# Performance work log

Measured on AMD Instinct MI355X. Metric: run time of the kernel, lower is better.

Reference implementation:

```python
import jax, jax.numpy as jnp
import numpy as np
import math

B, L, E, H = 4, 2048, 1024, 16
HD = E // H
SIGMA = 10.0
ATTN_BIAS = 0.1  # source bug: dropout_p=0.1 is passed as attn_mask and added to scores


def setup_inputs() -> dict:
    key = jax.random.key(0)
    ks = jax.random.split(key, 6)
    return {
        "query": jax.random.normal(ks[0], (B, L, E), jnp.float32),
        "key": jax.random.normal(ks[1], (B, L, E), jnp.float32),
        "value": jax.random.normal(ks[2], (B, L, E), jnp.float32),
        "gauss": jax.random.uniform(ks[3], (B * H // 2, L), jnp.float32),
        "in_proj_weight": jax.random.normal(ks[4], (3 * E, E), jnp.float32) * (1.0 / math.sqrt(E)),
        "in_proj_bias": jnp.zeros((3 * E,), jnp.float32),
        "out_proj_weight": jax.random.normal(ks[5], (E, E), jnp.float32) * (1.0 / math.sqrt(E)),
        "out_proj_bias": jnp.zeros((E,), jnp.float32),
    }


def reference(query, key, value, gauss, in_proj_weight, in_proj_bias,
              out_proj_weight, out_proj_bias):
    # packed in-projection (q,k,v distinct tensors -> chunk weights in 3)
    wq, wk, wv = jnp.split(in_proj_weight, 3, axis=0)   # each [E, E]
    bq, bk, bv = jnp.split(in_proj_bias, 3, axis=0)
    q = query @ wq.T + bq          # [B, L, E]
    k = key @ wk.T + bk
    v = value @ wv.T + bv

    def split_heads(x):            # [B, L, E] -> [B*H, L, HD], index = b*H + h
        return x.reshape(B, L, H, HD).transpose(0, 2, 1, 3).reshape(B * H, L, HD)

    q, k, v = split_heads(q), split_heads(k), split_heads(v)
    q = q * (1.0 / math.sqrt(HD))

    attn = jnp.einsum("bnd,bmd->bnm", q, k) + ATTN_BIAS   # [B*H, L, L]
    gw = jnp.exp(-gauss * SIGMA)                          # [B*H//2, L]
    # even/odd batch rows share the same gaussian row -> pairwise broadcast
    attn = (attn.reshape(B * H // 2, 2, L, L) * gw[:, None, None, :]).reshape(B * H, L, L)
    attn = jax.nn.softmax(attn, axis=-1)

    out = jnp.einsum("bnm,bmd->bnd", attn, v)             # [B*H, L, HD]
    out = out.reshape(B, H, L, HD).transpose(0, 2, 1, 3).reshape(B, L, E)
    return out @ out_proj_weight.T + out_proj_bias        # [B, L, E]
```

## Files before the change

### kernel.cpp

```cpp
#include <hip/hip_runtime.h>
#include <stdint.h>
#include <stddef.h>


typedef __attribute__((ext_vector_type(8))) short bf16x8;
typedef __attribute__((ext_vector_type(4))) float f32x4;
typedef __attribute__((ext_vector_type(8))) float f32x8;

__device__ __forceinline__ unsigned short f2b(float f) {
  unsigned int u = __builtin_bit_cast(unsigned int, f);
  u += 0x7FFFu + ((u >> 16) & 1u);
  return (unsigned short)(u >> 16);
}
__device__ __forceinline__ bf16x8 cvt8(f32x4 a, f32x4 b) {
  bf16x8 r;
#pragma unroll
  for (int i = 0; i < 4; ++i) { r[i] = (short)f2b(a[i]); r[4 + i] = (short)f2b(b[i]); }
  return r;
}
__device__ __forceinline__ bf16x8 pk8(f32x4 a, f32x4 b) {
  union { bf16x8 v; unsigned int w[4]; } u;
  asm("v_cvt_pk_bf16_f32 %0, %1, %2" : "=v"(u.w[0]) : "v"(a[0]), "v"(a[1]));
  asm("v_cvt_pk_bf16_f32 %0, %1, %2" : "=v"(u.w[1]) : "v"(a[2]), "v"(a[3]));
  asm("v_cvt_pk_bf16_f32 %0, %1, %2" : "=v"(u.w[2]) : "v"(b[0]), "v"(b[1]));
  asm("v_cvt_pk_bf16_f32 %0, %1, %2" : "=v"(u.w[3]) : "v"(b[2]), "v"(b[3]));
  return u.v;
}
__device__ __forceinline__ float fexp2(float x) { return __builtin_amdgcn_exp2f(x); }

#define GLD16(gp, lp) __builtin_amdgcn_global_load_lds( \
  (const __attribute__((address_space(1))) void*)(gp), \
  (__attribute__((address_space(3))) void*)(lp), 16, 0, 0)

__global__ void __launch_bounds__(256) gw_exp_kernel(const float* __restrict__ g,
                                                     float* __restrict__ gw2, int n) {
  int i = blockIdx.x * 256 + threadIdx.x;
  if (i < n) {
    const float e = __expf(g[i] * -10.0f) * 1.44269504f;
    gw2[2 * i] = e;
    gw2[2 * i + 1] = 0.1f * e;
  }
}

__global__ void __launch_bounds__(256) conv_bf16_kernel(
    const float* __restrict__ q, const float* __restrict__ k, const float* __restrict__ v,
    const float* __restrict__ w1, const float* __restrict__ w2,
    unsigned short* __restrict__ dst)
{
  const size_t i = ((size_t)blockIdx.x * 256 + threadIdx.x) * 8;
  const int seg = (int)(i >> 20);
  const float* s; size_t off;
  if (seg < 8)       { s = q;  off = i; }
  else if (seg < 16) { s = k;  off = i - ((size_t)8 << 20); }
  else if (seg < 24) { s = v;  off = i - ((size_t)16 << 20); }
  else if (seg < 27) { s = w1; off = i - ((size_t)24 << 20); }
  else               { s = w2; off = i - ((size_t)27 << 20); }
  const f32x4 a = *(const f32x4*)(s + off);
  const f32x4 b = *(const f32x4*)(s + off + 4);
  *(bf16x8*)(dst + i) = cvt8(a, b);
}

template<int EPI>
__global__ void __launch_bounds__(512) gemm_bt(
    const unsigned short* __restrict__ A0, const unsigned short* __restrict__ Bw,
    const float* __restrict__ bias,
    unsigned short* __restrict__ Qo, unsigned short* __restrict__ Ko,
    unsigned short* __restrict__ Vto, float* __restrict__ Co,
    int N, int K, int nTN)
{
  const int nwg = gridDim.x;
  const int cpx = nwg >> 3;
  const int bid2 = (blockIdx.x & 7) * cpx + (blockIdx.x >> 3);
  const int tm = bid2 / nTN, tn = bid2 % nTN;

  const unsigned short* A = A0;
  if (EPI == 0) A = A0 + (size_t)(tn >> 3) * 8388608;

  __shared__ __align__(16) char lds[3][16384];

  const int tid = threadIdx.x;
  const int w = tid >> 6, l = tid & 63;
  const int lr = l & 15, lg = l >> 4;
  const size_t Kz = (size_t)K;

  auto stage = [&](int buf, int kt) {
    const int k0 = kt * 32;
    const int rl = l >> 2;
    const int cs = (l & 3) ^ ((l >> 3) & 3);
    const size_t row = (size_t)(w * 16 + rl);
    GLD16(A  + Kz * (tm * 128 + row) + k0 + cs * 8, &lds[buf][w * 1024]);
    GLD16(Bw + Kz * (tn * 128 + row) + k0 + cs * 8, &lds[buf][8192 + w * 1024]);
  };

  auto loadFrag = [&](const char* ld, int row) -> bf16x8 {
    return *(const bf16x8*)(ld + row * 64 + ((lg ^ ((row >> 1) & 3)) << 4));
  };

  f32x4 acc[4][2];
  const f32x4 zero = {0.f, 0.f, 0.f, 0.f};
#pragma unroll
  for (int i = 0; i < 4; ++i)
#pragma unroll
    for (int j = 0; j < 2; ++j) acc[i][j] = zero;

  const int wr = (w >> 2) * 64, wc = (w & 3) * 32;
  const int NT = K / 32;

  stage(0, 0);
  stage(1, 1);
  int rb = 0, wb = 2;
  for (int kt = 0; kt < NT; ++kt) {
    if (kt == NT - 1) { asm volatile("s_waitcnt vmcnt(0)" ::: "memory"); }
    else              { asm volatile("s_waitcnt vmcnt(2)" ::: "memory"); }
    __builtin_amdgcn_sched_barrier(0);
    __builtin_amdgcn_s_barrier();
    __builtin_amdgcn_sched_barrier(0);
    if (kt + 2 < NT) stage(wb, kt + 2);
    const char* la = lds[rb];
    const char* lb = lds[rb] + 8192;
    bf16x8 af[4], bfr[2];
#pragma unroll
    for (int mi = 0; mi < 4; ++mi) af[mi] = loadFrag(la, wr + mi * 16 + lr);
#pragma unroll
    for (int ni = 0; ni < 2; ++ni) bfr[ni] = loadFrag(lb, wc + ni * 16 + lr);
#pragma unroll
    for (int mi = 0; mi < 4; ++mi)
#pragma unroll
      for (int ni = 0; ni < 2; ++ni)
        acc[mi][ni] = __builtin_amdgcn_mfma_f32_16x16x32_bf16(
            af[mi], bfr[ni], acc[mi][ni], 0, 0, 0);
    rb = (rb == 2) ? 0 : rb + 1;
    wb = (wb == 2) ? 0 : wb + 1;
  }

  if (EPI == 0 && tn >= 16) {
    __syncthreads();
    char* T = &lds[0][0];
#pragma unroll
    for (int ni = 0; ni < 2; ++ni) {
      const int cnl = wc + ni * 16 + lr;
      const float bv = bias[tn * 128 + cnl];
#pragma unroll
      for (int mi = 0; mi < 4; ++mi)
#pragma unroll
        for (int r = 0; r < 4; ++r) {
          const int rml = wr + mi * 16 + lg * 4 + r;
          const int byte = cnl * 256 + (((rml * 2)) ^ ((cnl & 3) << 5));
          *(unsigned short*)(T + byte) = f2b(acc[mi][ni][r] + bv);
        }
    }
    __syncthreads();
    const int bbase = (tm >> 4) * 16 + (tn - 16) * 2;
    const size_t ncol = (size_t)(tm & 15) * 128;
#pragma unroll
    for (int rep = 0; rep < 4; ++rep) {
      const int U = rep * 512 + tid;
      const int row = U >> 4;
      const int un = U & 15;
      const bf16x8 vv = *(const bf16x8*)(T + row * 256 + ((un * 16) ^ ((row & 3) << 5)));
      const int bh = bbase + (row >> 6);
      const int d = row & 63;
      *(bf16x8*)(Vto + ((size_t)bh * 64 + d) * 2048 + ncol + un * 8) = vv;
    }
  } else {
#pragma unroll
    for (int ni = 0; ni < 2; ++ni) {
      const int cn = tn * 128 + wc + ni * 16 + lr;
      const float bv = bias[cn];
#pragma unroll
      for (int mi = 0; mi < 4; ++mi) {
#pragma unroll
        for (int r = 0; r < 4; ++r) {
          const int rm = tm * 128 + wr + mi * 16 + lg * 4 + r;
          const float val = acc[mi][ni][r] + bv;
          if constexpr (EPI == 0) {
            const int which = cn >> 10;
            const int j = cn & 1023;
            const int bh = (rm >> 11) * 16 + (j >> 6);
            const int d = j & 63;
            const int n = rm & 2047;
            if (which == 0) Qo[((size_t)bh * 2048 + n) * 64 + d] = f2b(val * 0.125f);
            else            Ko[((size_t)bh * 2048 + n) * 64 + d] = f2b(val);
          } else {
            Co[(size_t)rm * N + cn] = val;
          }
        }
      }
    }
  }
}

__global__ void __launch_bounds__(256, 4) attn_kernel(
    const unsigned short* __restrict__ Q, const unsigned short* __restrict__ Kf,
    const unsigned short* __restrict__ Vt, const float* __restrict__ gw2,
    unsigned short* __restrict__ O)
{
  const int bh = blockIdx.x >> 4;
  const int qb = blockIdx.x & 15;
  const int tid = threadIdx.x;
  const int w = tid >> 6, l = tid & 63;
  const int lr = l & 15, lg = l >> 4;

  __shared__ __align__(16) unsigned short Kl[2][64 * 64];
  __shared__ __align__(16) unsigned short Vl[2][64 * 64];

  const int qrow = qb * 128 + w * 32 + lr;
  const unsigned short* qp = &Q[((size_t)bh * 2048 + qrow) * 64];
  const bf16x8 aqA0 = *(const bf16x8*)&qp[lg * 8];
  const bf16x8 aqA1 = *(const bf16x8*)&qp[32 + lg * 8];
  const bf16x8 aqB0 = *(const bf16x8*)&qp[16 * 64 + lg * 8];
  const bf16x8 aqB1 = *(const bf16x8*)&qp[16 * 64 + 32 + lg * 8];

  const f32x4 zero = {0.f, 0.f, 0.f, 0.f};
  f32x4 accOA[4], accOB[4], lA = zero, lB = zero;
#pragma unroll
  for (int dt = 0; dt < 4; ++dt) { accOA[dt] = zero; accOB[dt] = zero; }

  const short oneb = (short)0x3F80;
  const bf16x8 vones = {oneb, oneb, oneb, oneb, oneb, oneb, oneb, oneb};

  int off[4][2];
#pragma unroll
  for (int mt = 0; mt < 4; ++mt)
#pragma unroll
    for (int c = 0; c < 2; ++c) {
      const int rr = mt * 16 + lr;
      off[mt][c] = rr * 128 + ((((c << 2) + lg) ^ (rr & 7)) << 4);
    }

  const int rr0 = w * 8 + (l >> 3);
  const int cc = ((l & 7) ^ (rr0 & 7)) * 8;
  const int kk0 = (rr0 & 35) | ((rr0 & 12) << 1) | ((rr0 & 16) >> 2);
  const unsigned short* kSrc = &Kf[((size_t)bh * 2048 + kk0) * 64 + cc];
  const unsigned short* vSrc = &Vt[((size_t)bh * 64 + rr0) * 2048 + cc];

  auto stageKV = [&](int buf) {
    GLD16(kSrc,             &Kl[buf][w * 512]);
    GLD16(kSrc + 32 * 64,   &Kl[buf][(w + 4) * 512]);
    GLD16(vSrc,             &Vl[buf][w * 512]);
    GLD16(vSrc + 32 * 2048, &Vl[buf][(w + 4) * 512]);
    kSrc += 64 * 64;
    vSrc += 64;
  };

  const float* gwrow = &gw2[(size_t)(bh >> 1) * 4096];

  stageKV(0);
  for (int t = 0; t < 32; ++t) {
    __syncthreads();
    if (t + 1 < 32) stageKV((t + 1) & 1);
    const char* kl = (const char*)Kl[t & 1];
    const char* vl = (const char*)Vl[t & 1];

    f32x4 s0[4], s1[4];
    __builtin_amdgcn_s_setprio(1);
#pragma unroll
    for (int mt = 0; mt < 4; ++mt) {
      f32x4 a0 = zero, a1 = zero;
#pragma unroll
      for (int dk = 0; dk < 2; ++dk) {
        const bf16x8 bk = *(const bf16x8*)(kl + off[mt][dk]);
        a0 = __builtin_amdgcn_mfma_f32_16x16x32_bf16(bk, dk ? aqA1 : aqA0, a0, 0, 0, 0);
        a1 = __builtin_amdgcn_mfma_f32_16x16x32_bf16(bk, dk ? aqB1 : aqB0, a1, 0, 0, 0);
      }
      const f32x8 g8 = *(const f32x8*)(gwrow + ((t << 7) + ((mt >> 1) << 6) + ((mt & 1) << 3) + (lg << 4)));
#pragma unroll
      for (int r = 0; r < 4; ++r) {
        s0[mt][r] = __builtin_fmaf(a0[r], g8[2 * r], g8[2 * r + 1]);
        s1[mt][r] = __builtin_fmaf(a1[r], g8[2 * r], g8[2 * r + 1]);
      }
    }
    __builtin_amdgcn_s_setprio(0);

#pragma unroll
    for (int mt = 0; mt < 4; ++mt)
#pragma unroll
      for (int r = 0; r < 4; ++r) {
        s0[mt][r] = fexp2(s0[mt][r]);
        s1[mt][r] = fexp2(s1[mt][r]);
      }
    const bf16x8 apA0 = pk8(s0[0], s0[1]);
    const bf16x8 apA1 = pk8(s0[2], s0[3]);
    const bf16x8 apB0 = pk8(s1[0], s1[1]);
    const bf16x8 apB1 = pk8(s1[2], s1[3]);

    __builtin_amdgcn_s_setprio(1);
    lA = __builtin_amdgcn_mfma_f32_16x16x32_bf16(apA0, vones, lA, 0, 0, 0);
    lA = __builtin_amdgcn_mfma_f32_16x16x32_bf16(apA1, vones, lA, 0, 0, 0);
    lB = __builtin_amdgcn_mfma_f32_16x16x32_bf16(apB0, vones, lB, 0, 0, 0);
    lB = __builtin_amdgcn_mfma_f32_16x16x32_bf16(apB1, vones, lB, 0, 0, 0);

#pragma unroll
    for (int dt = 0; dt < 4; ++dt) {
      f32x4 a = accOA[dt], b = accOB[dt];
#pragma unroll
      for (int ms = 0; ms < 2; ++ms) {
        const bf16x8 bv = *(const bf16x8*)(vl + off[dt][ms]);
        a = __builtin_amdgcn_mfma_f32_16x16x32_bf16(ms ? apA1 : apA0, bv, a, 0, 0, 0);
        b = __builtin_amdgcn_mfma_f32_16x16x32_bf16(ms ? apB1 : apB0, bv, b, 0, 0, 0);
      }
      accOA[dt] = a; accOB[dt] = b;
    }
    __builtin_amdgcn_s_setprio(0);
  }

  const int orowA = (bh >> 4) * 2048 + qb * 128 + w * 32 + lg * 4;
  const int oc0 = (bh & 15) * 64;
  f32x4 rA, rB;
#pragma unroll
  for (int r = 0; r < 4; ++r) { rA[r] = 1.0f / lA[r]; rB[r] = 1.0f / lB[r]; }
#pragma unroll
  for (int dt = 0; dt < 4; ++dt) {
#pragma unroll
    for (int r = 0; r < 4; ++r) {
      O[(size_t)(orowA + r) * 1024 + oc0 + dt * 16 + lr]      = f2b(accOA[dt][r] * rA[r]);
      O[(size_t)(orowA + 16 + r) * 1024 + oc0 + dt * 16 + lr] = f2b(accOB[dt][r] * rB[r]);
    }
  }
}

extern "C" void kernel_launch(void* const* d_in, const int* in_sizes, int n_in,
                              void* d_out, int out_size, void* d_ws, size_t ws_size,
                              hipStream_t stream) {
  (void)in_sizes; (void)n_in; (void)out_size; (void)ws_size;
  const float* query = (const float*)d_in[0];
  const float* key_  = (const float*)d_in[1];
  const float* value = (const float*)d_in[2];
  const float* gauss = (const float*)d_in[3];
  const float* ipw   = (const float*)d_in[4];
  const float* ipb   = (const float*)d_in[5];
  const float* opw   = (const float*)d_in[6];
  const float* opb   = (const float*)d_in[7];

  char* ws = (char*)d_ws;
  unsigned short* Xbf = (unsigned short*)ws;
  unsigned short* W1  = Xbf + ((size_t)24 << 20);
  unsigned short* W2  = Xbf + ((size_t)27 << 20);
  unsigned short* AO  = Xbf;
  unsigned short* Qf  = Xbf + ((size_t)28 << 20);
  unsigned short* Kf  = Qf + (size_t)64 * 2048 * 64;
  unsigned short* Vt  = Kf + (size_t)64 * 2048 * 64;
  float*          gw2 = (float*)(Vt + (size_t)64 * 2048 * 64);

  gw_exp_kernel<<<256, 256, 0, stream>>>(gauss, gw2, 32 * 2048);

  conv_bf16_kernel<<<14336, 256, 0, stream>>>(query, key_, value, ipw, opw, Xbf);

  gemm_bt<0><<<64 * 24, 512, 0, stream>>>(
      Xbf, W1, ipb, Qf, Kf, Vt, nullptr, 3072, 1024, 24);

  attn_kernel<<<64 * 16, 256, 0, stream>>>(Qf, Kf, Vt, gw2, AO);

  gemm_bt<1><<<64 * 8, 512, 0, stream>>>(
      AO, W2, opb, nullptr, nullptr, nullptr, (float*)d_out, 1024, 1024, 8);
}
```

Baseline: 210.5 us.

## Fold gaussian scale into K projection and double attention rows per wave

The per-key gaussian weight (with log2e) is now multiplied into K inside the QKV projection epilogue, and the remaining additive bias is fed directly as the MFMA accumulator init. This removes the per-score FMA and interleaved table loads from the attention loop. Each wave now handles 64 query rows instead of 32, so every K/V fragment read from LDS is reused across four subtiles, with grid remapping and launch bounds lowered to 2 to allow the larger register footprint. The costs are more registers per thread, lower occupancy, and K rounded to bf16 after the gaussian scaling.

```diff
diff --git a/kernel.cpp b/kernel.cpp
--- a/kernel.cpp
+++ b/kernel.cpp
@@ -5,7 +5,6 @@
 
 typedef __attribute__((ext_vector_type(8))) short bf16x8;
 typedef __attribute__((ext_vector_type(4))) float f32x4;
-typedef __attribute__((ext_vector_type(8))) float f32x8;
 
 __device__ __forceinline__ unsigned short f2b(float f) {
   unsigned int u = __builtin_bit_cast(unsigned int, f);
@@ -33,12 +32,13 @@
   (__attribute__((address_space(3))) void*)(lp), 16, 0, 0)
 
 __global__ void __launch_bounds__(256) gw_exp_kernel(const float* __restrict__ g,
-                                                     float* __restrict__ gw2, int n) {
+                                                     float* __restrict__ gtab,
+                                                     float* __restrict__ btab, int n) {
   int i = blockIdx.x * 256 + threadIdx.x;
   if (i < n) {
     const float e = __expf(g[i] * -10.0f) * 1.44269504f;
-    gw2[2 * i] = e;
-    gw2[2 * i + 1] = 0.1f * e;
+    gtab[i] = e;
+    btab[i] = 0.1f * e;
   }
 }
 
@@ -63,7 +63,7 @@
 template<int EPI>
 __global__ void __launch_bounds__(512) gemm_bt(
     const unsigned short* __restrict__ A0, const unsigned short* __restrict__ Bw,
-    const float* __restrict__ bias,
+    const float* __restrict__ bias, const float* __restrict__ gtab,
     unsigned short* __restrict__ Qo, unsigned short* __restrict__ Ko,
     unsigned short* __restrict__ Vto, float* __restrict__ Co,
     int N, int K, int nTN)
@@ -167,20 +167,32 @@
     for (int ni = 0; ni < 2; ++ni) {
       const int cn = tn * 128 + wc + ni * 16 + lr;
       const float bv = bias[cn];
+      const int j = cn & 1023;
+      const float* gK = nullptr;
+      if constexpr (EPI == 0) {
+        if ((cn >> 10) == 1) {
+          const int bh_ = (tm >> 4) * 16 + (j >> 6);
+          gK = gtab + (size_t)(bh_ >> 1) * 2048;
+        }
+      }
 #pragma unroll
       for (int mi = 0; mi < 4; ++mi) {
+        const int rm0 = tm * 128 + wr + mi * 16 + lg * 4;
+        f32x4 g4;
+        if constexpr (EPI == 0) {
+          if (gK) g4 = *(const f32x4*)&gK[rm0 & 2047];
+        }
 #pragma unroll
         for (int r = 0; r < 4; ++r) {
-          const int rm = tm * 128 + wr + mi * 16 + lg * 4 + r;
+          const int rm = rm0 + r;
           const float val = acc[mi][ni][r] + bv;
           if constexpr (EPI == 0) {
             const int which = cn >> 10;
-            const int j = cn & 1023;
             const int bh = (rm >> 11) * 16 + (j >> 6);
             const int d = j & 63;
             const int n = rm & 2047;
             if (which == 0) Qo[((size_t)bh * 2048 + n) * 64 + d] = f2b(val * 0.125f);
-            else            Ko[((size_t)bh * 2048 + n) * 64 + d] = f2b(val);
+            else            Ko[((size_t)bh * 2048 + n) * 64 + d] = f2b(val * g4[r]);
           } else {
             Co[(size_t)rm * N + cn] = val;
           }
@@ -190,13 +202,14 @@
   }
 }
 
-__global__ void __launch_bounds__(256, 4) attn_kernel(
+__global__ void __launch_bounds__(256, 2) attn_kernel(
     const unsigned short* __restrict__ Q, const unsigned short* __restrict__ Kf,
-    const unsigned short* __restrict__ Vt, const float* __restrict__ gw2,
+    const unsigned short* __restrict__ Vt, const float* __restrict__ btab,
     unsigned short* __restrict__ O)
 {
-  const int bh = blockIdx.x >> 4;
-  const int qb = blockIdx.x & 15;
+  const int bid2 = (blockIdx.x & 7) * 64 + (blockIdx.x >> 3);
+  const int bh = bid2 >> 3;
+  const int qb = bid2 & 7;
   const int tid = threadIdx.x;
   const int w = tid >> 6, l = tid & 63;
   const int lr = l & 15, lg = l >> 4;
@@ -204,17 +217,24 @@
   __shared__ __align__(16) unsigned short Kl[2][64 * 64];
   __shared__ __align__(16) unsigned short Vl[2][64 * 64];
 
-  const int qrow = qb * 128 + w * 32 + lr;
+  const int qrow = qb * 256 + w * 64 + lr;
   const unsigned short* qp = &Q[((size_t)bh * 2048 + qrow) * 64];
-  const bf16x8 aqA0 = *(const bf16x8*)&qp[lg * 8];
-  const bf16x8 aqA1 = *(const bf16x8*)&qp[32 + lg * 8];
-  const bf16x8 aqB0 = *(const bf16x8*)&qp[16 * 64 + lg * 8];
-  const bf16x8 aqB1 = *(const bf16x8*)&qp[16 * 64 + 32 + lg * 8];
+  bf16x8 aq[4][2];
+#pragma unroll
+  for (int st = 0; st < 4; ++st) {
+    aq[st][0] = *(const bf16x8*)&qp[st * 16 * 64 + lg * 8];
+    aq[st][1] = *(const bf16x8*)&qp[st * 16 * 64 + 32 + lg * 8];
+  }
 
   const f32x4 zero = {0.f, 0.f, 0.f, 0.f};
-  f32x4 accOA[4], accOB[4], lA = zero, lB = zero;
-#pragma unroll
-  for (int dt = 0; dt < 4; ++dt) { accOA[dt] = zero; accOB[dt] = zero; }
+  f32x4 accO[4][4];
+  f32x4 lsum[4];
+#pragma unroll
+  for (int st = 0; st < 4; ++st) {
+    lsum[st] = zero;
+#pragma unroll
+    for (int dt = 0; dt < 4; ++dt) accO[st][dt] = zero;
+  }
 
   const short oneb = (short)0x3F80;
   const bf16x8 vones = {oneb, oneb, oneb, oneb, oneb, oneb, oneb, oneb};
@@ -243,7 +263,7 @@
     vSrc += 64;
   };
 
-  const float* gwrow = &gw2[(size_t)(bh >> 1) * 4096];
+  const float* brow = &btab[(size_t)(bh >> 1) * 2048];
 
   stageKV(0);
   for (int t = 0; t < 32; ++t) {
@@ -252,70 +272,68 @@
     const char* kl = (const char*)Kl[t & 1];
     const char* vl = (const char*)Vl[t & 1];
 
-    f32x4 s0[4], s1[4];
+    bf16x8 ap[4][2];
+#pragma unroll
+    for (int half = 0; half < 2; ++half) {
+      f32x4 s[4][2];
+      __builtin_amdgcn_s_setprio(1);
+#pragma unroll
+      for (int mh = 0; mh < 2; ++mh) {
+        const int mt = half * 2 + mh;
+        const bf16x8 bk0 = *(const bf16x8*)(kl + off[mt][0]);
+        const bf16x8 bk1 = *(const bf16x8*)(kl + off[mt][1]);
+        const f32x4 b4 = *(const f32x4*)&brow[t * 64 + (half << 5) + (lg << 3) + (mh << 2)];
+#pragma unroll
+        for (int st = 0; st < 4; ++st) {
+          f32x4 a = __builtin_amdgcn_mfma_f32_16x16x32_bf16(bk0, aq[st][0], b4, 0, 0, 0);
+          a = __builtin_amdgcn_mfma_f32_16x16x32_bf16(bk1, aq[st][1], a, 0, 0, 0);
+          s[st][mh] = a;
+        }
+      }
+      __builtin_amdgcn_s_setprio(0);
+#pragma unroll
+      for (int st = 0; st < 4; ++st) {
+#pragma unroll
+        for (int mh = 0; mh < 2; ++mh)
+#pragma unroll
+          for (int r = 0; r < 4; ++r) s[st][mh][r] = fexp2(s[st][mh][r]);
+        ap[st][half] = pk8(s[st][0], s[st][1]);
+      }
+    }
+
     __builtin_amdgcn_s_setprio(1);
 #pragma unroll
-    for (int mt = 0; mt < 4; ++mt) {
-      f32x4 a0 = zero, a1 = zero;
-#pragma unroll
-      for (int dk = 0; dk < 2; ++dk) {
-        const bf16x8 bk = *(const bf16x8*)(kl + off[mt][dk]);
-        a0 = __builtin_amdgcn_mfma_f32_16x16x32_bf16(bk, dk ? aqA1 : aqA0, a0, 0, 0, 0);
-        a1 = __builtin_amdgcn_mfma_f32_16x16x32_bf16(bk, dk ? aqB1 : aqB0, a1, 0, 0, 0);
-      }
-      const f32x8 g8 = *(const f32x8*)(gwrow + ((t << 7) + ((mt >> 1) << 6) + ((mt & 1) << 3) + (lg << 4)));
-#pragma unroll
-      for (int r = 0; r < 4; ++r) {
-        s0[mt][r] = __builtin_fmaf(a0[r], g8[2 * r], g8[2 * r + 1]);
-        s1[mt][r] = __builtin_fmaf(a1[r], g8[2 * r], g8[2 * r + 1]);
+    for (int st = 0; st < 4; ++st) {
+      lsum[st] = __builtin_amdgcn_mfma_f32_16x16x32_bf16(ap[st][0], vones, lsum[st], 0, 0, 0);
+      lsum[st] = __builtin_amdgcn_mfma_f32_16x16x32_bf16(ap[st][1], vones, lsum[st], 0, 0, 0);
+    }
+#pragma unroll
+    for (int dt = 0; dt < 4; ++dt) {
+      const bf16x8 bv0 = *(const bf16x8*)(vl + off[dt][0]);
+      const bf16x8 bv1 = *(const bf16x8*)(vl + off[dt][1]);
+#pragma unroll
+      for (int st = 0; st < 4; ++st) {
+        f32x4 a = accO[st][dt];
+        a = __builtin_amdgcn_mfma_f32_16x16x32_bf16(ap[st][0], bv0, a, 0, 0, 0);
+        a = __builtin_amdgcn_mfma_f32_16x16x32_bf16(ap[st][1], bv1, a, 0, 0, 0);
+        accO[st][dt] = a;
       }
     }
     __builtin_amdgcn_s_setprio(0);
-
-#pragma unroll
-    for (int mt = 0; mt < 4; ++mt)
-#pragma unroll
-      for (int r = 0; r < 4; ++r) {
-        s0[mt][r] = fexp2(s0[mt][r]);
-        s1[mt][r] = fexp2(s1[mt][r]);
-      }
-    const bf16x8 apA0 = pk8(s0[0], s0[1]);
-    const bf16x8 apA1 = pk8(s0[2], s0[3]);
-    const bf16x8 apB0 = pk8(s1[0], s1[1]);
-    const bf16x8 apB1 = pk8(s1[2], s1[3]);
-
-    __builtin_amdgcn_s_setprio(1);
-    lA = __builtin_amdgcn_mfma_f32_16x16x32_bf16(apA0, vones, lA, 0, 0, 0);
-    lA = __builtin_amdgcn_mfma_f32_16x16x32_bf16(apA1, vones, lA, 0, 0, 0);
-    lB = __builtin_amdgcn_mfma_f32_16x16x32_bf16(apB0, vones, lB, 0, 0, 0);
-    lB = __builtin_amdgcn_mfma_f32_16x16x32_bf16(apB1, vones, lB, 0, 0, 0);
-
-#pragma unroll
-    for (int dt = 0; dt < 4; ++dt) {
-      f32x4 a = accOA[dt], b = accOB[dt];
-#pragma unroll
-      for (int ms = 0; ms < 2; ++ms) {
-        const bf16x8 bv = *(const bf16x8*)(vl + off[dt][ms]);
-        a = __builtin_amdgcn_mfma_f32_16x16x32_bf16(ms ? apA1 : apA0, bv, a, 0, 0, 0);
-        b = __builtin_amdgcn_mfma_f32_16x16x32_bf16(ms ? apB1 : apB0, bv, b, 0, 0, 0);
-      }
-      accOA[dt] = a; accOB[dt] = b;
-    }
-    __builtin_amdgcn_s_setprio(0);
-  }
-
-  const int orowA = (bh >> 4) * 2048 + qb * 128 + w * 32 + lg * 4;
+  }
+
   const int oc0 = (bh & 15) * 64;
-  f32x4 rA, rB;
-#pragma unroll
-  for (int r = 0; r < 4; ++r) { rA[r] = 1.0f / lA[r]; rB[r] = 1.0f / lB[r]; }
-#pragma unroll
-  for (int dt = 0; dt < 4; ++dt) {
-#pragma unroll
-    for (int r = 0; r < 4; ++r) {
-      O[(size_t)(orowA + r) * 1024 + oc0 + dt * 16 + lr]      = f2b(accOA[dt][r] * rA[r]);
-      O[(size_t)(orowA + 16 + r) * 1024 + oc0 + dt * 16 + lr] = f2b(accOB[dt][r] * rB[r]);
-    }
+#pragma unroll
+  for (int st = 0; st < 4; ++st) {
+    const int orow0 = (bh >> 4) * 2048 + qb * 256 + w * 64 + st * 16 + lg * 4;
+    f32x4 rc;
+#pragma unroll
+    for (int r = 0; r < 4; ++r) rc[r] = 1.0f / lsum[st][r];
+#pragma unroll
+    for (int dt = 0; dt < 4; ++dt)
+#pragma unroll
+      for (int r = 0; r < 4; ++r)
+        O[(size_t)(orow0 + r) * 1024 + oc0 + dt * 16 + lr] = f2b(accO[st][dt][r] * rc[r]);
   }
 }
 
@@ -340,17 +358,18 @@
   unsigned short* Qf  = Xbf + ((size_t)28 << 20);
   unsigned short* Kf  = Qf + (size_t)64 * 2048 * 64;
   unsigned short* Vt  = Kf + (size_t)64 * 2048 * 64;
-  float*          gw2 = (float*)(Vt + (size_t)64 * 2048 * 64);
-
-  gw_exp_kernel<<<256, 256, 0, stream>>>(gauss, gw2, 32 * 2048);
+  float*          gtab = (float*)(Vt + (size_t)64 * 2048 * 64);
+  float*          btab = gtab + 32 * 2048;
+
+  gw_exp_kernel<<<256, 256, 0, stream>>>(gauss, gtab, btab, 32 * 2048);
 
   conv_bf16_kernel<<<14336, 256, 0, stream>>>(query, key_, value, ipw, opw, Xbf);
 
   gemm_bt<0><<<64 * 24, 512, 0, stream>>>(
-      Xbf, W1, ipb, Qf, Kf, Vt, nullptr, 3072, 1024, 24);
-
-  attn_kernel<<<64 * 16, 256, 0, stream>>>(Qf, Kf, Vt, gw2, AO);
+      Xbf, W1, ipb, gtab, Qf, Kf, Vt, nullptr, 3072, 1024, 24);
+
+  attn_kernel<<<512, 256, 0, stream>>>(Qf, Kf, Vt, btab, AO);
 
   gemm_bt<1><<<64 * 8, 512, 0, stream>>>(
-      AO, W2, opb, nullptr, nullptr, nullptr, (float*)d_out, 1024, 1024, 8);
-}
+      AO, W2, opb, nullptr, nullptr, nullptr, nullptr, (float*)d_out, 1024, 1024, 8);
+}
```

After: 204.9 us. 2.6% less time.
